# Optimization experiments

Hardware: AMD Instinct MI355X
Metric: run time of the kernel (lower is better)

The kernel has to match this reference:

```python
import jax, jax.numpy as jnp
import numpy as np

H = 50000   # hidden_size
IN = 50000  # in_size
NNZ = 800000
B = 8
T = 32


def spmm(indices, values, num_rows, x):
    """COO sparse @ dense. indices: (2, nnz) int, values: (nnz,), x: (K, N)."""
    rows, cols = indices[0], indices[1]
    contrib = values[:, None] * x[cols]          # (nnz, N) gather + scale
    return jax.ops.segment_sum(contrib, rows, num_segments=num_rows)  # (M, N)


def setup_inputs() -> dict:
    key = jax.random.key(0)
    k1, k2, k3, k4, k5 = jax.random.split(key, 5)
    x = jax.random.normal(k1, (B, T, IN), dtype=jnp.float32)
    hh_indices = jax.random.randint(k2, (2, NNZ), 0, H)
    hh_values = jax.random.normal(k3, (NNZ,), dtype=jnp.float32) * 0.1
    hh_bias = jnp.zeros((H, 1), dtype=jnp.float32)
    ih_indices = jax.random.randint(k4, (2, NNZ), 0, IN)
    ih_values = jax.random.normal(k5, (NNZ,), dtype=jnp.float32) * 0.1
    return {"x": x, "hh_values": hh_values, "hh_bias": hh_bias,
            "ih_values": ih_values, "hh_indices": hh_indices,
            "ih_indices": ih_indices}


def reference(x, hh_values, hh_bias, ih_values, hh_indices, ih_indices):
    # x: (B, T, IN) batch_first -> (T, IN, B) as in _format_x
    xt = jnp.transpose(x, (1, 2, 0))
    h0 = jnp.zeros((H, x.shape[0]), dtype=x.dtype)  # zeros init, (H, B)

    def step(h, x_t):
        pre = (spmm(hh_indices, hh_values, H, h) + hh_bias
               + spmm(ih_indices, ih_values, H, x_t))
        h_new = jnp.tanh(pre)  # layernorm is Identity (use_layernorm=False)
        return h_new, h_new

    _, hs = jax.lax.scan(step, h0, xt)       # (T, H, B)
    return jnp.transpose(hs, (2, 0, 1))      # (B, T, H) batch_first
```

## Files before the change

kernel.cpp:

```cpp
#include <hip/hip_runtime.h>
#include <math.h>

#define HSZ 50000
#define INSZ 50000
#define NNZc 800000
#define BSZ 8
#define TSZ 32

#define CHUNK 2048
#define NBLK ((NNZc + CHUNK - 1) / CHUNK)
#define NCB 196
#define HWORDS (256 * NBLK)
#define NC2 ((HWORDS + 1023) / 1024)

typedef _Float16 half8 __attribute__((ext_vector_type(8)));
typedef _Float16 half4 __attribute__((ext_vector_type(4)));

__device__ __forceinline__ unsigned f2h_bits(float f) {
    _Float16 h = (_Float16)f;
    unsigned short u;
    __builtin_memcpy(&u, &h, 2);
    return (unsigned)u;
}
__device__ __forceinline__ float h_bits2f(unsigned u) {
    unsigned short us = (unsigned short)u;
    _Float16 h;
    __builtin_memcpy(&h, &us, 2);
    return (float)h;
}


__global__ void p1_count(const int* __restrict__ hh_idx, const int* __restrict__ ih_idx,
                         int* __restrict__ ghist) {
    const int* rows = blockIdx.y ? ih_idx : hh_idx;
    __shared__ int cnt[256];
    int tid = threadIdx.x;
    cnt[tid] = 0;
    __syncthreads();
    int base = blockIdx.x * CHUNK;
    int nElem = min(CHUNK, NNZc - base);
    for (int k = tid; k < nElem; k += 256) {
        atomicAdd(&cnt[rows[base + k] >> 8], 1);
    }
    __syncthreads();
    ghist[((size_t)blockIdx.y * 256 + tid) * NBLK + blockIdx.x] = cnt[tid];
}

__global__ void p2scanA(int* __restrict__ ghist, int* __restrict__ partials) {
    int* g = ghist + (size_t)blockIdx.y * HWORDS;
    __shared__ int sm[1024];
    int tid = threadIdx.x;
    int idx = blockIdx.x * 1024 + tid;
    int v = (idx < HWORDS) ? g[idx] : 0;
    sm[tid] = v;
    __syncthreads();
    int x = v;
    for (int off = 1; off < 1024; off <<= 1) {
        int y = (tid >= off) ? sm[tid - off] : 0;
        __syncthreads();
        x += y;
        sm[tid] = x;
        __syncthreads();
    }
    if (idx < HWORDS) g[idx] = x - v;
    if (tid == 1023) partials[blockIdx.y * 128 + blockIdx.x] = x;
}

__global__ void p2scanB(int* __restrict__ partials) {
    __shared__ int sm[128];
    int tid = threadIdx.x;
    for (int m = 0; m < 2; ++m) {
        int v = (tid < NC2) ? partials[m * 128 + tid] : 0;
        sm[tid] = v;
        __syncthreads();
        int x = v;
        for (int off = 1; off < 128; off <<= 1) {
            int y = (tid >= off) ? sm[tid - off] : 0;
            __syncthreads();
            x += y;
            sm[tid] = x;
            __syncthreads();
        }
        if (tid < NC2) partials[m * 128 + tid] = x - v;
        __syncthreads();
    }
}

__global__ void p2scanC(int* __restrict__ ghist, const int* __restrict__ partials,
                        int* __restrict__ cbs) {
    int mat = blockIdx.y;
    int* g = ghist + (size_t)mat * HWORDS;
    int i = blockIdx.x * 256 + threadIdx.x;
    if (i < HWORDS) {
        int v = g[i] + partials[mat * 128 + (i >> 10)];
        g[i] = v;
        int b = i / NBLK;
        if (i - b * NBLK == 0 && b < NCB) cbs[mat * (NCB + 1) + b] = v;
    }
    if (i == 0) cbs[mat * (NCB + 1) + NCB] = NNZc;
}

__global__ void p2_part(const int* __restrict__ hh_idx, const float* __restrict__ hh_v,
                        const int* __restrict__ ih_idx, const float* __restrict__ ih_v,
                        const int* __restrict__ ghist,
                        uint2* __restrict__ tmp_hh, uint2* __restrict__ tmp_ih) {
    int mat = blockIdx.y;
    const int* idx = mat ? ih_idx : hh_idx;
    const float* val = mat ? ih_v : hh_v;
    uint2* tmp = mat ? tmp_ih : tmp_hh;
    const int* g = ghist + (size_t)mat * HWORDS;

    __shared__ int cnt[256];
    __shared__ int lstart[256];
    __shared__ int scanbuf[256];
    __shared__ int gbase[256];
    __shared__ uint2 stage[CHUNK];

    int tid = threadIdx.x;
    int base = blockIdx.x * CHUNK;
    int nElem = min(CHUNK, NNZc - base);

    cnt[tid] = 0;
    gbase[tid] = g[(size_t)tid * NBLK + blockIdx.x];
    __syncthreads();
    for (int k = tid; k < nElem; k += 256) {
        atomicAdd(&cnt[idx[base + k] >> 8], 1);
    }
    __syncthreads();
    int v = cnt[tid];
    scanbuf[tid] = v;
    __syncthreads();
    int x = v;
    for (int off = 1; off < 256; off <<= 1) {
        int y = (tid >= off) ? scanbuf[tid - off] : 0;
        __syncthreads();
        x += y;
        scanbuf[tid] = x;
        __syncthreads();
    }
    lstart[tid] = x - v;
    cnt[tid] = 0;
    __syncthreads();
    for (int k = tid; k < nElem; k += 256) {
        int r = idx[base + k];
        int c = idx[NNZc + base + k];
        int b = r >> 8;
        int rank = atomicAdd(&cnt[b], 1);
        stage[lstart[b] + rank] = make_uint2(((unsigned)r << 16) | (unsigned)c,
                                             __float_as_uint(val[base + k]));
    }
    __syncthreads();
    for (int k = tid; k < nElem; k += 256) {
        uint2 el = stage[k];
        int b = el.x >> 24;
        tmp[gbase[b] + (k - lstart[b])] = el;
    }
}

__global__ void p3_final(const int* __restrict__ cbs,
                         const uint2* __restrict__ tmp_hh, const uint2* __restrict__ tmp_ih,
                         int* __restrict__ ptr_hh, int* __restrict__ ptr_ih,
                         unsigned* __restrict__ cv_hh, unsigned* __restrict__ cv_ih) {
    int mat = blockIdx.y;
    const uint2* tmp = mat ? tmp_ih : tmp_hh;
    int* ptr = mat ? ptr_ih : ptr_hh;
    unsigned* cv = mat ? cv_ih : cv_hh;
    __shared__ int rcnt[256];
    __shared__ int rstart[256];
    __shared__ int scanbuf[256];
    int cb = blockIdx.x;
    int row0 = cb << 8;
    int nrows = min(256, HSZ - row0);
    int s = cbs[mat * (NCB + 1) + cb];
    int e = cbs[mat * (NCB + 1) + cb + 1];
    int tid = threadIdx.x;
    rcnt[tid] = 0;
    __syncthreads();
    for (int k = s + tid; k < e; k += 256) {
        atomicAdd(&rcnt[(tmp[k].x >> 16) & 255], 1);
    }
    __syncthreads();
    int v = rcnt[tid];
    scanbuf[tid] = v;
    __syncthreads();
    int x = v;
    for (int off = 1; off < 256; off <<= 1) {
        int y = (tid >= off) ? scanbuf[tid - off] : 0;
        __syncthreads();
        x += y;
        scanbuf[tid] = x;
        __syncthreads();
    }
    rstart[tid] = x - v;
    if (tid < nrows) ptr[row0 + tid] = s + x - v;
    if (cb == NCB - 1 && tid == 0) ptr[HSZ] = NNZc;
    rcnt[tid] = 0;
    __syncthreads();
    for (int k = s + tid; k < e; k += 256) {
        uint2 el = tmp[k];
        int lr = (el.x >> 16) & 255;
        int rank = atomicAdd(&rcnt[lr], 1);
        cv[s + rstart[lr] + rank] =
            (f2h_bits(__uint_as_float(el.y)) << 16) | (el.x & 0xffffu);
    }
}


__global__ void transpose_x2(const float* __restrict__ x, _Float16* __restrict__ X2h) {
    extern __shared__ float tile[];
    int i0 = blockIdx.x * 64;
    int tid = threadIdx.x;
    int il = tid & 15;
    int tr = (tid >> 4) & 3;
    int tg = tid >> 6;
#pragma unroll
    for (int iter = 0; iter < 16; ++iter) {
        int tb = iter * 16 + tg * 4 + tr;
        int t = tb >> 3, b = tb & 7;
        const float4 v = *reinterpret_cast<const float4*>(
            x + ((size_t)b * TSZ + t) * INSZ + i0 + il * 4);
        tile[(il * 4 + 0) * 257 + tb] = v.x;
        tile[(il * 4 + 1) * 257 + tb] = v.y;
        tile[(il * 4 + 2) * 257 + tb] = v.z;
        tile[(il * 4 + 3) * 257 + tb] = v.w;
    }
    __syncthreads();
    for (int k = 0; k < 64; ++k) {
        int i = i0 + k;
        if (i < INSZ) X2h[(size_t)i * 256 + tid] = (_Float16)tile[k * 257 + tid];
    }
}


__global__ void ihc_kernel(const int* __restrict__ ptr, const unsigned* __restrict__ cv,
                           const float* __restrict__ bias, const half4* __restrict__ X2h,
                           half4* __restrict__ ihcT) {
    __shared__ half4 lds[4 * 65];
    int wid = threadIdx.x >> 6;
    int lane = threadIdx.x & 63;
    int r = (blockIdx.x << 2) + wid;
    int s = ptr[r], e = ptr[r + 1];
    s = __builtin_amdgcn_readfirstlane(s);
    e = __builtin_amdgcn_readfirstlane(e);
    float4 acc = make_float4(0.f, 0.f, 0.f, 0.f);
    int j = s;
    for (; j + 1 < e; j += 2) {
        unsigned a = cv[j], b = cv[j + 1];
        float va = h_bits2f(a >> 16);
        float vb = h_bits2f(b >> 16);
        half4 x0 = X2h[((size_t)(a & 0xffffu) << 6) + lane];
        half4 x1 = X2h[((size_t)(b & 0xffffu) << 6) + lane];
        acc.x = fmaf(va, (float)x0[0], acc.x);
        acc.y = fmaf(va, (float)x0[1], acc.y);
        acc.z = fmaf(va, (float)x0[2], acc.z);
        acc.w = fmaf(va, (float)x0[3], acc.w);
        acc.x = fmaf(vb, (float)x1[0], acc.x);
        acc.y = fmaf(vb, (float)x1[1], acc.y);
        acc.z = fmaf(vb, (float)x1[2], acc.z);
        acc.w = fmaf(vb, (float)x1[3], acc.w);
    }
    if (j < e) {
        unsigned a = cv[j];
        float va = h_bits2f(a >> 16);
        half4 x0 = X2h[((size_t)(a & 0xffffu) << 6) + lane];
        acc.x = fmaf(va, (float)x0[0], acc.x);
        acc.y = fmaf(va, (float)x0[1], acc.y);
        acc.z = fmaf(va, (float)x0[2], acc.z);
        acc.w = fmaf(va, (float)x0[3], acc.w);
    }
    float bb = bias[r];
    half4 o;
    o[0] = (_Float16)(acc.x + bb);
    o[1] = (_Float16)(acc.y + bb);
    o[2] = (_Float16)(acc.z + bb);
    o[3] = (_Float16)(acc.w + bb);
    lds[wid * 65 + lane] = o;
    __syncthreads();
    int plane = threadIdx.x >> 3;
    int w = threadIdx.x & 7;
    int row = w >> 1, q = w & 1;
    int r2 = (blockIdx.x << 2) + row;
    ihcT[((size_t)plane * HSZ + r2) * 2 + q] = lds[row * 65 + 2 * plane + q];
}


__device__ __forceinline__ float fast_tanh(float x) {
    float e = __expf(2.0f * x);
    return 1.0f - __fdividef(2.0f, e + 1.0f);
}

__global__ void step_kernel(const int* __restrict__ ptr, const unsigned* __restrict__ cv,
                            const half8* __restrict__ ihcT, const half8* __restrict__ h_in,
                            half8* __restrict__ h_out, float* __restrict__ out, int t) {
    int gid = blockIdx.x * 256 + threadIdx.x;
    if (gid >= 4 * HSZ) return;
    int sub = gid & 3;
    int r = gid >> 2;
    int s = ptr[r], e = ptr[r + 1];
    half8 base8 = ihcT[(size_t)t * HSZ + r];
    float acc0 = 0.f, acc1 = 0.f, acc2 = 0.f, acc3 = 0.f;
    float acc4 = 0.f, acc5 = 0.f, acc6 = 0.f, acc7 = 0.f;
    for (int j = s + sub; j < e; j += 4) {
        unsigned u = cv[j];
        float v = h_bits2f(u >> 16);
        half8 hv = h_in[u & 0xffffu];
        acc0 = fmaf(v, (float)hv[0], acc0);
        acc1 = fmaf(v, (float)hv[1], acc1);
        acc2 = fmaf(v, (float)hv[2], acc2);
        acc3 = fmaf(v, (float)hv[3], acc3);
        acc4 = fmaf(v, (float)hv[4], acc4);
        acc5 = fmaf(v, (float)hv[5], acc5);
        acc6 = fmaf(v, (float)hv[6], acc6);
        acc7 = fmaf(v, (float)hv[7], acc7);
    }
    acc0 += __shfl_xor(acc0, 1); acc1 += __shfl_xor(acc1, 1);
    acc2 += __shfl_xor(acc2, 1); acc3 += __shfl_xor(acc3, 1);
    acc4 += __shfl_xor(acc4, 1); acc5 += __shfl_xor(acc5, 1);
    acc6 += __shfl_xor(acc6, 1); acc7 += __shfl_xor(acc7, 1);
    acc0 += __shfl_xor(acc0, 2); acc1 += __shfl_xor(acc1, 2);
    acc2 += __shfl_xor(acc2, 2); acc3 += __shfl_xor(acc3, 2);
    acc4 += __shfl_xor(acc4, 2); acc5 += __shfl_xor(acc5, 2);
    acc6 += __shfl_xor(acc6, 2); acc7 += __shfl_xor(acc7, 2);
    if (sub == 0) {
        float h0 = fast_tanh(acc0 + (float)base8[0]);
        float h1 = fast_tanh(acc1 + (float)base8[1]);
        float h2 = fast_tanh(acc2 + (float)base8[2]);
        float h3 = fast_tanh(acc3 + (float)base8[3]);
        float h4 = fast_tanh(acc4 + (float)base8[4]);
        float h5 = fast_tanh(acc5 + (float)base8[5]);
        float h6 = fast_tanh(acc6 + (float)base8[6]);
        float h7 = fast_tanh(acc7 + (float)base8[7]);
        half8 hh;
        hh[0] = (_Float16)h0; hh[1] = (_Float16)h1;
        hh[2] = (_Float16)h2; hh[3] = (_Float16)h3;
        hh[4] = (_Float16)h4; hh[5] = (_Float16)h5;
        hh[6] = (_Float16)h6; hh[7] = (_Float16)h7;
        h_out[r] = hh;
        out[((size_t)0 * TSZ + t) * HSZ + r] = h0;
        out[((size_t)1 * TSZ + t) * HSZ + r] = h1;
        out[((size_t)2 * TSZ + t) * HSZ + r] = h2;
        out[((size_t)3 * TSZ + t) * HSZ + r] = h3;
        out[((size_t)4 * TSZ + t) * HSZ + r] = h4;
        out[((size_t)5 * TSZ + t) * HSZ + r] = h5;
        out[((size_t)6 * TSZ + t) * HSZ + r] = h6;
        out[((size_t)7 * TSZ + t) * HSZ + r] = h7;
    }
}


static inline size_t align256(size_t x) { return (x + 255) & ~(size_t)255; }

extern "C" void kernel_launch(void* const* d_in, const int* in_sizes, int n_in,
                              void* d_out, int out_size, void* d_ws, size_t ws_size,
                              hipStream_t stream) {
    const float* x          = (const float*)d_in[0];
    const float* hh_values  = (const float*)d_in[1];
    const float* hh_bias    = (const float*)d_in[2];
    const float* ih_values  = (const float*)d_in[3];
    const int*   hh_indices = (const int*)d_in[4];
    const int*   ih_indices = (const int*)d_in[5];
    float* out = (float*)d_out;

    char* ws = (char*)d_ws;
    _Float16* X2h   = (_Float16*)ws; ws += align256((size_t)INSZ * 256 * 2);
    half4*  ihcT    = (half4*)ws;  ws += align256((size_t)HSZ * 256 * 2);
    half8*  hbuf    = (half8*)ws;  ws += align256((size_t)2 * HSZ * 16);
    int*    hh_ptr  = (int*)ws;    ws += align256((size_t)(HSZ + 1) * 4);
    int*    ih_ptr  = (int*)ws;    ws += align256((size_t)(HSZ + 1) * 4);
    int*    ghist   = (int*)ws;    ws += align256((size_t)2 * HWORDS * 4);
    int*    partials= (int*)ws;    ws += align256((size_t)256 * 4);
    int*    cbs     = (int*)ws;    ws += align256((size_t)2 * (NCB + 1) * 4);
    uint2*  tmp_hh  = (uint2*)ws;  ws += align256((size_t)NNZc * 8);
    uint2*  tmp_ih  = (uint2*)ws;  ws += align256((size_t)NNZc * 8);
    unsigned* cv_hh = (unsigned*)ws; ws += align256((size_t)NNZc * 4);
    unsigned* cv_ih = (unsigned*)ws; ws += align256((size_t)NNZc * 4);

    hipMemsetAsync(hbuf, 0, (size_t)HSZ * 16, stream);

    p1_count<<<dim3(NBLK, 2), 256, 0, stream>>>(hh_indices, ih_indices, ghist);
    p2scanA<<<dim3(NC2, 2), 1024, 0, stream>>>(ghist, partials);
    p2scanB<<<1, 128, 0, stream>>>(partials);
    p2scanC<<<dim3((HWORDS + 255) / 256, 2), 256, 0, stream>>>(ghist, partials, cbs);
    p2_part<<<dim3(NBLK, 2), 256, 0, stream>>>(hh_indices, hh_values, ih_indices, ih_values,
                                               ghist, tmp_hh, tmp_ih);
    p3_final<<<dim3(NCB, 2), 256, 0, stream>>>(cbs, tmp_hh, tmp_ih,
                                               hh_ptr, ih_ptr, cv_hh, cv_ih);

    transpose_x2<<<(INSZ + 63) / 64, 256, 64 * 257 * 4, stream>>>(x, X2h);
    ihc_kernel<<<HSZ / 4, 256, 0, stream>>>(ih_ptr, cv_ih, hh_bias, (const half4*)X2h, ihcT);

    int stepBlocks = (4 * HSZ + 255) / 256;
    for (int t = 0; t < TSZ; ++t) {
        half8* hin  = hbuf + (size_t)(t & 1) * HSZ;
        half8* hout = hbuf + (size_t)((t + 1) & 1) * HSZ;
        step_kernel<<<stepBlocks, 256, 0, stream>>>(hh_ptr, cv_hh, (const half8*)ihcT,
                                                    hin, hout, out, t);
    }
}
```

Baseline: 507.6 us.

## Split ih SpMM by column slices and defer fp32 output expansion to one pass

The ih precompute kernel is restructured so that each block handles 16 rows and one of eight column slices. Each thread packs two half values per 32-bit load, which spreads work across more blocks and lets results be written directly in the transposed layout without an LDS staging step. The recurrent step kernel no longer writes eight scattered fp32 output values per row per step. It stores fp16 hidden states for all timesteps into a history buffer that reuses the X2h workspace, and a final kernel expands that history to the fp32 output. The t=0 step skips the hh SpMM instead of reading a zeroed buffer, which removes the memset, but the fp32 output now carries fp16 rounding.

```diff
diff --git a/kernel.cpp b/kernel.cpp
--- a/kernel.cpp
+++ b/kernel.cpp
@@ -232,55 +232,42 @@
 }
 
 
-__global__ void ihc_kernel(const int* __restrict__ ptr, const unsigned* __restrict__ cv,
-                           const float* __restrict__ bias, const half4* __restrict__ X2h,
-                           half4* __restrict__ ihcT) {
-    __shared__ half4 lds[4 * 65];
-    int wid = threadIdx.x >> 6;
-    int lane = threadIdx.x & 63;
-    int r = (blockIdx.x << 2) + wid;
-    int s = ptr[r], e = ptr[r + 1];
-    s = __builtin_amdgcn_readfirstlane(s);
-    e = __builtin_amdgcn_readfirstlane(e);
-    float4 acc = make_float4(0.f, 0.f, 0.f, 0.f);
-    int j = s;
-    for (; j + 1 < e; j += 2) {
-        unsigned a = cv[j], b = cv[j + 1];
-        float va = h_bits2f(a >> 16);
-        float vb = h_bits2f(b >> 16);
-        half4 x0 = X2h[((size_t)(a & 0xffffu) << 6) + lane];
-        half4 x1 = X2h[((size_t)(b & 0xffffu) << 6) + lane];
-        acc.x = fmaf(va, (float)x0[0], acc.x);
-        acc.y = fmaf(va, (float)x0[1], acc.y);
-        acc.z = fmaf(va, (float)x0[2], acc.z);
-        acc.w = fmaf(va, (float)x0[3], acc.w);
-        acc.x = fmaf(vb, (float)x1[0], acc.x);
-        acc.y = fmaf(vb, (float)x1[1], acc.y);
-        acc.z = fmaf(vb, (float)x1[2], acc.z);
-        acc.w = fmaf(vb, (float)x1[3], acc.w);
-    }
-    if (j < e) {
-        unsigned a = cv[j];
-        float va = h_bits2f(a >> 16);
-        half4 x0 = X2h[((size_t)(a & 0xffffu) << 6) + lane];
-        acc.x = fmaf(va, (float)x0[0], acc.x);
-        acc.y = fmaf(va, (float)x0[1], acc.y);
-        acc.z = fmaf(va, (float)x0[2], acc.z);
-        acc.w = fmaf(va, (float)x0[3], acc.w);
+__global__ void ihc_kernel2(const int* __restrict__ ptr, const unsigned* __restrict__ cv,
+                            const float* __restrict__ bias, const unsigned* __restrict__ X2u,
+                            unsigned* __restrict__ ihcU) {
+    int s = blockIdx.x & 7;
+    int rb = blockIdx.x >> 3;
+    int tid = threadIdx.x;
+    int r = rb * 16 + (tid >> 4);
+    int l = tid & 15;
+    int cbase = s * 16 + l;
+    int js = ptr[r], je = ptr[r + 1];
+    float a0 = 0.f, a1 = 0.f;
+    int j = js;
+    for (; j + 1 < je; j += 2) {
+        unsigned u0 = cv[j], u1 = cv[j + 1];
+        float v0 = h_bits2f(u0 >> 16);
+        float v1 = h_bits2f(u1 >> 16);
+        unsigned p0 = X2u[((size_t)(u0 & 0xffffu) << 7) + cbase];
+        unsigned p1 = X2u[((size_t)(u1 & 0xffffu) << 7) + cbase];
+        a0 = fmaf(v0, h_bits2f(p0 & 0xffffu), a0);
+        a1 = fmaf(v0, h_bits2f(p0 >> 16), a1);
+        a0 = fmaf(v1, h_bits2f(p1 & 0xffffu), a0);
+        a1 = fmaf(v1, h_bits2f(p1 >> 16), a1);
+    }
+    if (j < je) {
+        unsigned u0 = cv[j];
+        float v0 = h_bits2f(u0 >> 16);
+        unsigned p0 = X2u[((size_t)(u0 & 0xffffu) << 7) + cbase];
+        a0 = fmaf(v0, h_bits2f(p0 & 0xffffu), a0);
+        a1 = fmaf(v0, h_bits2f(p0 >> 16), a1);
     }
     float bb = bias[r];
-    half4 o;
-    o[0] = (_Float16)(acc.x + bb);
-    o[1] = (_Float16)(acc.y + bb);
-    o[2] = (_Float16)(acc.z + bb);
-    o[3] = (_Float16)(acc.w + bb);
-    lds[wid * 65 + lane] = o;
-    __syncthreads();
-    int plane = threadIdx.x >> 3;
-    int w = threadIdx.x & 7;
-    int row = w >> 1, q = w & 1;
-    int r2 = (blockIdx.x << 2) + row;
-    ihcT[((size_t)plane * HSZ + r2) * 2 + q] = lds[row * 65 + 2 * plane + q];
+    unsigned o = f2h_bits(a0 + bb) | (f2h_bits(a1 + bb) << 16);
+    int c0 = cbase << 1;
+    int t = c0 >> 3;
+    int b0 = c0 & 7;
+    ihcU[((size_t)t * HSZ + r) * 4 + (b0 >> 1)] = o;
 }
 
 
@@ -290,28 +277,29 @@
 }
 
 __global__ void step_kernel(const int* __restrict__ ptr, const unsigned* __restrict__ cv,
-                            const half8* __restrict__ ihcT, const half8* __restrict__ h_in,
-                            half8* __restrict__ h_out, float* __restrict__ out, int t) {
+                            const half8* __restrict__ ihcT, half8* __restrict__ hs, int t) {
     int gid = blockIdx.x * 256 + threadIdx.x;
     if (gid >= 4 * HSZ) return;
     int sub = gid & 3;
     int r = gid >> 2;
     int s = ptr[r], e = ptr[r + 1];
-    half8 base8 = ihcT[(size_t)t * HSZ + r];
+    const half8* __restrict__ h_in = hs + (size_t)(t - 1) * HSZ;
     float acc0 = 0.f, acc1 = 0.f, acc2 = 0.f, acc3 = 0.f;
     float acc4 = 0.f, acc5 = 0.f, acc6 = 0.f, acc7 = 0.f;
-    for (int j = s + sub; j < e; j += 4) {
-        unsigned u = cv[j];
-        float v = h_bits2f(u >> 16);
-        half8 hv = h_in[u & 0xffffu];
-        acc0 = fmaf(v, (float)hv[0], acc0);
-        acc1 = fmaf(v, (float)hv[1], acc1);
-        acc2 = fmaf(v, (float)hv[2], acc2);
-        acc3 = fmaf(v, (float)hv[3], acc3);
-        acc4 = fmaf(v, (float)hv[4], acc4);
-        acc5 = fmaf(v, (float)hv[5], acc5);
-        acc6 = fmaf(v, (float)hv[6], acc6);
-        acc7 = fmaf(v, (float)hv[7], acc7);
+    if (t > 0) {
+        for (int j = s + sub; j < e; j += 4) {
+            unsigned u = cv[j];
+            float v = h_bits2f(u >> 16);
+            half8 hv = h_in[u & 0xffffu];
+            acc0 = fmaf(v, (float)hv[0], acc0);
+            acc1 = fmaf(v, (float)hv[1], acc1);
+            acc2 = fmaf(v, (float)hv[2], acc2);
+            acc3 = fmaf(v, (float)hv[3], acc3);
+            acc4 = fmaf(v, (float)hv[4], acc4);
+            acc5 = fmaf(v, (float)hv[5], acc5);
+            acc6 = fmaf(v, (float)hv[6], acc6);
+            acc7 = fmaf(v, (float)hv[7], acc7);
+        }
     }
     acc0 += __shfl_xor(acc0, 1); acc1 += __shfl_xor(acc1, 1);
     acc2 += __shfl_xor(acc2, 1); acc3 += __shfl_xor(acc3, 1);
@@ -322,29 +310,29 @@
     acc4 += __shfl_xor(acc4, 2); acc5 += __shfl_xor(acc5, 2);
     acc6 += __shfl_xor(acc6, 2); acc7 += __shfl_xor(acc7, 2);
     if (sub == 0) {
-        float h0 = fast_tanh(acc0 + (float)base8[0]);
-        float h1 = fast_tanh(acc1 + (float)base8[1]);
-        float h2 = fast_tanh(acc2 + (float)base8[2]);
-        float h3 = fast_tanh(acc3 + (float)base8[3]);
-        float h4 = fast_tanh(acc4 + (float)base8[4]);
-        float h5 = fast_tanh(acc5 + (float)base8[5]);
-        float h6 = fast_tanh(acc6 + (float)base8[6]);
-        float h7 = fast_tanh(acc7 + (float)base8[7]);
+        half8 base8 = ihcT[(size_t)t * HSZ + r];
         half8 hh;
-        hh[0] = (_Float16)h0; hh[1] = (_Float16)h1;
-        hh[2] = (_Float16)h2; hh[3] = (_Float16)h3;
-        hh[4] = (_Float16)h4; hh[5] = (_Float16)h5;
-        hh[6] = (_Float16)h6; hh[7] = (_Float16)h7;
-        h_out[r] = hh;
-        out[((size_t)0 * TSZ + t) * HSZ + r] = h0;
-        out[((size_t)1 * TSZ + t) * HSZ + r] = h1;
-        out[((size_t)2 * TSZ + t) * HSZ + r] = h2;
-        out[((size_t)3 * TSZ + t) * HSZ + r] = h3;
-        out[((size_t)4 * TSZ + t) * HSZ + r] = h4;
-        out[((size_t)5 * TSZ + t) * HSZ + r] = h5;
-        out[((size_t)6 * TSZ + t) * HSZ + r] = h6;
-        out[((size_t)7 * TSZ + t) * HSZ + r] = h7;
-    }
+        hh[0] = (_Float16)fast_tanh(acc0 + (float)base8[0]);
+        hh[1] = (_Float16)fast_tanh(acc1 + (float)base8[1]);
+        hh[2] = (_Float16)fast_tanh(acc2 + (float)base8[2]);
+        hh[3] = (_Float16)fast_tanh(acc3 + (float)base8[3]);
+        hh[4] = (_Float16)fast_tanh(acc4 + (float)base8[4]);
+        hh[5] = (_Float16)fast_tanh(acc5 + (float)base8[5]);
+        hh[6] = (_Float16)fast_tanh(acc6 + (float)base8[6]);
+        hh[7] = (_Float16)fast_tanh(acc7 + (float)base8[7]);
+        hs[(size_t)t * HSZ + r] = hh;
+    }
+}
+
+
+__global__ void expand_out(const half8* __restrict__ hs, float* __restrict__ out) {
+    int gid = blockIdx.x * 256 + threadIdx.x;
+    int t = gid / HSZ;
+    int r = gid - t * HSZ;
+    half8 h = hs[gid];
+#pragma unroll
+    for (int b = 0; b < 8; ++b)
+        out[((size_t)b * TSZ + t) * HSZ + r] = (float)h[b];
 }
 
 
@@ -363,8 +351,8 @@
 
     char* ws = (char*)d_ws;
     _Float16* X2h   = (_Float16*)ws; ws += align256((size_t)INSZ * 256 * 2);
+    half8*  hs      = (half8*)X2h;
     half4*  ihcT    = (half4*)ws;  ws += align256((size_t)HSZ * 256 * 2);
-    half8*  hbuf    = (half8*)ws;  ws += align256((size_t)2 * HSZ * 16);
     int*    hh_ptr  = (int*)ws;    ws += align256((size_t)(HSZ + 1) * 4);
     int*    ih_ptr  = (int*)ws;    ws += align256((size_t)(HSZ + 1) * 4);
     int*    ghist   = (int*)ws;    ws += align256((size_t)2 * HWORDS * 4);
@@ -375,8 +363,6 @@
     unsigned* cv_hh = (unsigned*)ws; ws += align256((size_t)NNZc * 4);
     unsigned* cv_ih = (unsigned*)ws; ws += align256((size_t)NNZc * 4);
 
-    hipMemsetAsync(hbuf, 0, (size_t)HSZ * 16, stream);
-
     p1_count<<<dim3(NBLK, 2), 256, 0, stream>>>(hh_indices, ih_indices, ghist);
     p2scanA<<<dim3(NC2, 2), 1024, 0, stream>>>(ghist, partials);
     p2scanB<<<1, 128, 0, stream>>>(partials);
@@ -387,13 +373,14 @@
                                                hh_ptr, ih_ptr, cv_hh, cv_ih);
 
     transpose_x2<<<(INSZ + 63) / 64, 256, 64 * 257 * 4, stream>>>(x, X2h);
-    ihc_kernel<<<HSZ / 4, 256, 0, stream>>>(ih_ptr, cv_ih, hh_bias, (const half4*)X2h, ihcT);
+    ihc_kernel2<<<dim3((HSZ / 16) * 8), 256, 0, stream>>>(ih_ptr, cv_ih, hh_bias,
+                                                          (const unsigned*)X2h,
+                                                          (unsigned*)ihcT);
 
     int stepBlocks = (4 * HSZ + 255) / 256;
     for (int t = 0; t < TSZ; ++t) {
-        half8* hin  = hbuf + (size_t)(t & 1) * HSZ;
-        half8* hout = hbuf + (size_t)((t + 1) & 1) * HSZ;
         step_kernel<<<stepBlocks, 256, 0, stream>>>(hh_ptr, cv_hh, (const half8*)ihcT,
-                                                    hin, hout, out, t);
-    }
-}
+                                                    hs, t);
+    }
+    expand_out<<<(TSZ * HSZ) / 256, 256, 0, stream>>>((const half8*)hs, out);
+}
```

After: 568.5 us. 12.0% more time.

## Store hidden history in fp16 buffer, widen row split to 8, expand output at end

Applied to the files above, without the earlier changes.

The step kernel now writes each timestep's hidden state only as packed fp16 into a history buffer that reuses the X2h workspace. A single expand_out kernel converts it to the fp32 (B,T,H) output after the loop, replacing the strided per-step fp32 stores. Each row is now split across 8 lanes instead of 4, with an extra shuffle stage, and the t=0 step skips the recurrent SpMV instead of relying on a memset of the initial state. This trades one extra pass over the output for cheaper, more parallel step kernels.

```diff
diff --git a/kernel.cpp b/kernel.cpp
--- a/kernel.cpp
+++ b/kernel.cpp
@@ -290,28 +290,29 @@
 }
 
 __global__ void step_kernel(const int* __restrict__ ptr, const unsigned* __restrict__ cv,
-                            const half8* __restrict__ ihcT, const half8* __restrict__ h_in,
-                            half8* __restrict__ h_out, float* __restrict__ out, int t) {
+                            const half8* __restrict__ ihcT, half8* __restrict__ hs, int t) {
     int gid = blockIdx.x * 256 + threadIdx.x;
-    if (gid >= 4 * HSZ) return;
-    int sub = gid & 3;
-    int r = gid >> 2;
+    if (gid >= 8 * HSZ) return;
+    int sub = gid & 7;
+    int r = gid >> 3;
     int s = ptr[r], e = ptr[r + 1];
-    half8 base8 = ihcT[(size_t)t * HSZ + r];
+    const half8* __restrict__ h_in = hs + (size_t)(t - 1) * HSZ;
     float acc0 = 0.f, acc1 = 0.f, acc2 = 0.f, acc3 = 0.f;
     float acc4 = 0.f, acc5 = 0.f, acc6 = 0.f, acc7 = 0.f;
-    for (int j = s + sub; j < e; j += 4) {
-        unsigned u = cv[j];
-        float v = h_bits2f(u >> 16);
-        half8 hv = h_in[u & 0xffffu];
-        acc0 = fmaf(v, (float)hv[0], acc0);
-        acc1 = fmaf(v, (float)hv[1], acc1);
-        acc2 = fmaf(v, (float)hv[2], acc2);
-        acc3 = fmaf(v, (float)hv[3], acc3);
-        acc4 = fmaf(v, (float)hv[4], acc4);
-        acc5 = fmaf(v, (float)hv[5], acc5);
-        acc6 = fmaf(v, (float)hv[6], acc6);
-        acc7 = fmaf(v, (float)hv[7], acc7);
+    if (t > 0) {
+        for (int j = s + sub; j < e; j += 8) {
+            unsigned u = cv[j];
+            float v = h_bits2f(u >> 16);
+            half8 hv = h_in[u & 0xffffu];
+            acc0 = fmaf(v, (float)hv[0], acc0);
+            acc1 = fmaf(v, (float)hv[1], acc1);
+            acc2 = fmaf(v, (float)hv[2], acc2);
+            acc3 = fmaf(v, (float)hv[3], acc3);
+            acc4 = fmaf(v, (float)hv[4], acc4);
+            acc5 = fmaf(v, (float)hv[5], acc5);
+            acc6 = fmaf(v, (float)hv[6], acc6);
+            acc7 = fmaf(v, (float)hv[7], acc7);
+        }
     }
     acc0 += __shfl_xor(acc0, 1); acc1 += __shfl_xor(acc1, 1);
     acc2 += __shfl_xor(acc2, 1); acc3 += __shfl_xor(acc3, 1);
@@ -321,30 +322,34 @@
     acc2 += __shfl_xor(acc2, 2); acc3 += __shfl_xor(acc3, 2);
     acc4 += __shfl_xor(acc4, 2); acc5 += __shfl_xor(acc5, 2);
     acc6 += __shfl_xor(acc6, 2); acc7 += __shfl_xor(acc7, 2);
+    acc0 += __shfl_xor(acc0, 4); acc1 += __shfl_xor(acc1, 4);
+    acc2 += __shfl_xor(acc2, 4); acc3 += __shfl_xor(acc3, 4);
+    acc4 += __shfl_xor(acc4, 4); acc5 += __shfl_xor(acc5, 4);
+    acc6 += __shfl_xor(acc6, 4); acc7 += __shfl_xor(acc7, 4);
     if (sub == 0) {
-        float h0 = fast_tanh(acc0 + (float)base8[0]);
-        float h1 = fast_tanh(acc1 + (float)base8[1]);
-        float h2 = fast_tanh(acc2 + (float)base8[2]);
-        float h3 = fast_tanh(acc3 + (float)base8[3]);
-        float h4 = fast_tanh(acc4 + (float)base8[4]);
-        float h5 = fast_tanh(acc5 + (float)base8[5]);
-        float h6 = fast_tanh(acc6 + (float)base8[6]);
-        float h7 = fast_tanh(acc7 + (float)base8[7]);
+        half8 base8 = ihcT[(size_t)t * HSZ + r];
         half8 hh;
-        hh[0] = (_Float16)h0; hh[1] = (_Float16)h1;
-        hh[2] = (_Float16)h2; hh[3] = (_Float16)h3;
-        hh[4] = (_Float16)h4; hh[5] = (_Float16)h5;
-        hh[6] = (_Float16)h6; hh[7] = (_Float16)h7;
-        h_out[r] = hh;
-        out[((size_t)0 * TSZ + t) * HSZ + r] = h0;
-        out[((size_t)1 * TSZ + t) * HSZ + r] = h1;
-        out[((size_t)2 * TSZ + t) * HSZ + r] = h2;
-        out[((size_t)3 * TSZ + t) * HSZ + r] = h3;
-        out[((size_t)4 * TSZ + t) * HSZ + r] = h4;
-        out[((size_t)5 * TSZ + t) * HSZ + r] = h5;
-        out[((size_t)6 * TSZ + t) * HSZ + r] = h6;
-        out[((size_t)7 * TSZ + t) * HSZ + r] = h7;
-    }
+        hh[0] = (_Float16)fast_tanh(acc0 + (float)base8[0]);
+        hh[1] = (_Float16)fast_tanh(acc1 + (float)base8[1]);
+        hh[2] = (_Float16)fast_tanh(acc2 + (float)base8[2]);
+        hh[3] = (_Float16)fast_tanh(acc3 + (float)base8[3]);
+        hh[4] = (_Float16)fast_tanh(acc4 + (float)base8[4]);
+        hh[5] = (_Float16)fast_tanh(acc5 + (float)base8[5]);
+        hh[6] = (_Float16)fast_tanh(acc6 + (float)base8[6]);
+        hh[7] = (_Float16)fast_tanh(acc7 + (float)base8[7]);
+        hs[(size_t)t * HSZ + r] = hh;
+    }
+}
+
+
+__global__ void expand_out(const half8* __restrict__ hs, float* __restrict__ out) {
+    int gid = blockIdx.x * 256 + threadIdx.x;
+    int t = gid / HSZ;
+    int r = gid - t * HSZ;
+    half8 h = hs[gid];
+#pragma unroll
+    for (int b = 0; b < 8; ++b)
+        out[((size_t)b * TSZ + t) * HSZ + r] = (float)h[b];
 }
 
 
@@ -363,8 +368,8 @@
 
     char* ws = (char*)d_ws;
     _Float16* X2h   = (_Float16*)ws; ws += align256((size_t)INSZ * 256 * 2);
+    half8*  hs      = (half8*)X2h;
     half4*  ihcT    = (half4*)ws;  ws += align256((size_t)HSZ * 256 * 2);
-    half8*  hbuf    = (half8*)ws;  ws += align256((size_t)2 * HSZ * 16);
     int*    hh_ptr  = (int*)ws;    ws += align256((size_t)(HSZ + 1) * 4);
     int*    ih_ptr  = (int*)ws;    ws += align256((size_t)(HSZ + 1) * 4);
     int*    ghist   = (int*)ws;    ws += align256((size_t)2 * HWORDS * 4);
@@ -375,8 +380,6 @@
     unsigned* cv_hh = (unsigned*)ws; ws += align256((size_t)NNZc * 4);
     unsigned* cv_ih = (unsigned*)ws; ws += align256((size_t)NNZc * 4);
 
-    hipMemsetAsync(hbuf, 0, (size_t)HSZ * 16, stream);
-
     p1_count<<<dim3(NBLK, 2), 256, 0, stream>>>(hh_indices, ih_indices, ghist);
     p2scanA<<<dim3(NC2, 2), 1024, 0, stream>>>(ghist, partials);
     p2scanB<<<1, 128, 0, stream>>>(partials);
@@ -389,11 +392,10 @@
     transpose_x2<<<(INSZ + 63) / 64, 256, 64 * 257 * 4, stream>>>(x, X2h);
     ihc_kernel<<<HSZ / 4, 256, 0, stream>>>(ih_ptr, cv_ih, hh_bias, (const half4*)X2h, ihcT);
 
-    int stepBlocks = (4 * HSZ + 255) / 256;
+    int stepBlocks = (8 * HSZ + 255) / 256;
     for (int t = 0; t < TSZ; ++t) {
-        half8* hin  = hbuf + (size_t)(t & 1) * HSZ;
-        half8* hout = hbuf + (size_t)((t + 1) & 1) * HSZ;
         step_kernel<<<stepBlocks, 256, 0, stream>>>(hh_ptr, cv_hh, (const half8*)ihcT,
-                                                    hin, hout, out, t);
-    }
-}
+                                                    hs, t);
+    }
+    expand_out<<<(TSZ * HSZ) / 256, 256, 0, stream>>>((const half8*)hs, out);
+}
```

Result: slower. 522.3 us (+2.9%).
